# Optimization experiments

Hardware: AMD Instinct MI355X
Metric: run time of the kernel (lower is better)

The kernel has to match this reference:

```python
import jax, jax.numpy as jnp
import numpy as np

N_NODES = 50000
N_REL = 1000
N_EDGES = 1600000
F_OUT = 64
N_HEAD = 2
NEG_SLOPE = 0.2


def setup_inputs() -> dict:
    key = jax.random.key(0)
    k_h, k_r, k_a0, k_a1, k_a2, k_w, k_att = jax.random.split(key, 7)
    h = jax.random.normal(k_h, (N_NODES, F_OUT), dtype=jnp.float32)
    inputr = jax.random.normal(k_r, (N_REL, F_OUT), dtype=jnp.float32)
    # A[0]=dst node, A[1]=relation id, A[2]=src node
    a0 = jax.random.randint(k_a0, (N_EDGES,), 0, N_NODES, dtype=jnp.int32)
    a1 = jax.random.randint(k_a1, (N_EDGES,), 0, N_REL, dtype=jnp.int32)
    a2 = jax.random.randint(k_a2, (N_EDGES,), 0, N_NODES, dtype=jnp.int32)
    A = jnp.stack([a0, a1, a2], axis=0)
    # params: w ~ diag per-head scale, a_src_dst ~ N(0, 1/sqrt(2*f_out))
    w = jax.random.normal(k_w, (N_HEAD - 1, 1, F_OUT), dtype=jnp.float32)
    stdv = 1.0 / np.sqrt(2 * F_OUT)
    a_src_dst = (jax.random.normal(k_att, (N_HEAD, 2, F_OUT, 1), dtype=jnp.float32) * stdv)
    return {"h": h, "inputr": inputr, "A": A, "w": w, "a_src_dst": a_src_dst}


def reference(h, inputr, A, w, a_src_dst):
    N = h.shape[0]
    dst, rel_idx, src_idx = A[0], A[1], A[2]
    outs = []
    for i in range(N_HEAD):
        if i >= 1:
            h = h * w[i - 1]  # cumulative diag rescale across heads
        src = h[src_idx]          # [E, f] gather
        rel = inputr[rel_idx]     # [E, f] gather
        score = src @ a_src_dst[i, 0] + rel @ a_src_dst[i, 1]  # [E, 1]
        edge_e = jnp.exp(-jax.nn.leaky_relu(score[:, 0], NEG_SLOPE))  # [E]
        rowsum = jax.ops.segment_sum(edge_e, dst, num_segments=N)[:, None]  # [N,1]
        msg = (src - rel) * edge_e[:, None]  # [E, f]
        h_prime = jax.ops.segment_sum(msg, dst, num_segments=N) / rowsum
        outs.append(h_prime)
    return jnp.stack(outs, axis=0)  # [n_head, N, f]
```

## Files before the change

kernel.cpp:

```cpp
#include <hip/hip_runtime.h>
#include <hip/hip_fp16.h>

#define NNODES 50000
#define NREL   1000
#define NEDGES 1600000
#define FOUT   64
#define NEG_SLOPE 0.2f

#define SPAN   32
#define NBUCK  1563
#define CAP    1280
#define PTHR   1024
#define EPT    16
#define CHUNK  (PTHR * EPT)
#define DBLK   98
#define PREB   797


#define ALIGN1K(x) (((x) + 1023) & ~((size_t)1023))
static const size_t OFF_HS    = 0;
static const size_t OFF_RR    = ALIGN1K(OFF_HS    + sizeof(float2) * NNODES);
static const size_t OFF_CNT   = ALIGN1K(OFF_RR    + sizeof(float2) * NREL);
static const size_t OFF_H16   = ALIGN1K(OFF_CNT   + sizeof(int) * NBUCK);
static const size_t OFF_R16   = ALIGN1K(OFF_H16   + sizeof(unsigned short) * NNODES * FOUT);
static const size_t OFF_STAGE = ALIGN1K(OFF_R16   + sizeof(unsigned short) * NREL * FOUT);

__global__ __launch_bounds__(PTHR) void prep_kernel(
    const float* __restrict__ h, const float* __restrict__ inputr,
    const float* __restrict__ w, const float* __restrict__ a_att,
    const int* __restrict__ A, int* __restrict__ ccnt, int* __restrict__ stage,
    float2* __restrict__ hs2, float2* __restrict__ rr2,
    unsigned short* __restrict__ h16, unsigned short* __restrict__ r16)
{
    const int t = threadIdx.x;
    if (blockIdx.x < DBLK) {
        __shared__ int lcnt[NBUCK];
        __shared__ int gbase[NBUCK];
        for (int i = t; i < NBUCK; i += PTHR) lcnt[i] = 0;
        __syncthreads();

        const int base = blockIdx.x * CHUNK;
        int rec[EPT];
        short bkt[EPT];
        int off[EPT];

        #pragma unroll
        for (int k = 0; k < EPT; k++) {
            const int e = base + k * PTHR + t;
            if (e < NEDGES) {
                const int dn = __builtin_nontemporal_load(A + e);
                const int rn = __builtin_nontemporal_load(A + NEDGES + e);
                const int sn = __builtin_nontemporal_load(A + 2 * NEDGES + e);
                const int b  = dn >> 5;
                rec[k] = ((dn & 31) << 26) | (sn << 10) | rn;
                bkt[k] = (short)b;
                off[k] = atomicAdd(&lcnt[b], 1);
            } else {
                off[k] = -1;
            }
        }
        __syncthreads();

        for (int i = t; i < NBUCK; i += PTHR) {
            const int c = lcnt[i];
            if (c > 0) gbase[i] = i * CAP + atomicAdd(&ccnt[i], c);
        }
        __syncthreads();

        #pragma unroll
        for (int k = 0; k < EPT; k++) {
            if (off[k] >= 0) {
                const int b   = bkt[k];
                const int pos = gbase[b] + off[k];
                if (pos < (b + 1) * CAP)
                    stage[pos] = rec[k];
            }
        }
        return;
    }

    const int lane = t & 15;
    const int f0   = lane << 2;
    const int g    = (blockIdx.x - DBLK) * 64 + (t >> 4);
    if (g >= NNODES + NREL) return;

    const float4 a00 = *(const float4*)(a_att +   0 + f0);
    const float4 a01 = *(const float4*)(a_att +  64 + f0);
    const float4 a10 = *(const float4*)(a_att + 128 + f0);
    const float4 a11 = *(const float4*)(a_att + 192 + f0);
    const float4 wv  = *(const float4*)(w + f0);

    float p0, p1;
    float4 v;
    if (g < NNODES) {
        v = *(const float4*)(h + (size_t)g * FOUT + f0);
        p0 = v.x * a00.x + v.y * a00.y + v.z * a00.z + v.w * a00.w;
        p1 = v.x * wv.x * a10.x + v.y * wv.y * a10.y
           + v.z * wv.z * a10.z + v.w * wv.w * a10.w;
    } else {
        v = *(const float4*)(inputr + (size_t)(g - NNODES) * FOUT + f0);
        p0 = v.x * a01.x + v.y * a01.y + v.z * a01.z + v.w * a01.w;
        p1 = v.x * a11.x + v.y * a11.y + v.z * a11.z + v.w * a11.w;
    }

    {
        ushort4 pk;
        pk.x = __half_as_ushort(__float2half(v.x));
        pk.y = __half_as_ushort(__float2half(v.y));
        pk.z = __half_as_ushort(__float2half(v.z));
        pk.w = __half_as_ushort(__float2half(v.w));
        if (g < NNODES) *(ushort4*)(h16 + (size_t)g * FOUT + f0) = pk;
        else            *(ushort4*)(r16 + (size_t)(g - NNODES) * FOUT + f0) = pk;
    }

    #pragma unroll
    for (int off = 8; off >= 1; off >>= 1) {
        p0 += __shfl_xor(p0, off, 16);
        p1 += __shfl_xor(p1, off, 16);
    }
    if (lane == 0) {
        if (g < NNODES) hs2[g] = make_float2(p0, p1);
        else            rr2[g - NNODES] = make_float2(p0, p1);
    }
}

__global__ __launch_bounds__(256) void sortagg_kernel(
    const unsigned short* __restrict__ h16, const unsigned short* __restrict__ r16,
    const float* __restrict__ w,
    const int* __restrict__ stage, const int* __restrict__ ccnt,
    const float2* __restrict__ hs2, const float2* __restrict__ rr2,
    float* __restrict__ out)
{
    __shared__ int    lsort[CAP];
    __shared__ float2 ew[CAP];
    __shared__ int hist[SPAN];
    __shared__ int offs[SPAN];
    __shared__ int sstart[SPAN + 1];

    const int b = blockIdx.x;
    const int t = threadIdx.x;
    int cnt = ccnt[b];
    if (cnt > CAP) cnt = CAP;
    const int base = b * CAP;

    if (t < SPAN) hist[t] = 0;
    __syncthreads();

    for (int i = t; i < cnt; i += 256)
        atomicAdd(&hist[((unsigned)stage[base + i]) >> 26], 1);
    __syncthreads();

    if (t < SPAN) {
        const int c = hist[t];
        int v = c;
        #pragma unroll
        for (int d = 1; d < SPAN; d <<= 1) {
            const int u = __shfl_up(v, d);
            if (t >= d) v += u;
        }
        sstart[t] = v - c;
        offs[t]   = v - c;
        if (t == SPAN - 1) sstart[SPAN] = v;
    }
    __syncthreads();

    for (int i = t; i < cnt; i += 256) {
        const int r = stage[base + i];
        const int pos = atomicAdd(&offs[((unsigned)r) >> 26], 1);
        lsort[pos] = r;
        const int sn = (r >> 10) & 0xFFFF;
        const int rn = r & 1023;
        const float2 hv = hs2[sn];
        const float2 rv = rr2[rn];
        const float sc0 = hv.x + rv.x;
        const float sc1 = hv.y + rv.y;
        ew[pos] = make_float2(__expf(-fmaxf(sc0, NEG_SLOPE * sc0)),
                              __expf(-fmaxf(sc1, NEG_SLOPE * sc1)));
    }
    __syncthreads();

    const int wv = t >> 6;
    const int q  = (t & 63) >> 4;
    const int f4 = (t & 15) << 2;
    const float4 wl = *(const float4*)(w + f4);

    for (int nl = wv; nl < SPAN; nl += 4) {
        const int node = b * SPAN + nl;
        if (node >= NNODES) break;
        const int s0 = sstart[nl];
        const int s1 = sstart[nl + 1];

        float4 acc0 = make_float4(0.f, 0.f, 0.f, 0.f);
        float4 acc1 = make_float4(0.f, 0.f, 0.f, 0.f);
        float sum0 = 0.f, sum1 = 0.f;

        for (int i = s0 + q; i < s1; i += 4) {
            const int p     = lsort[i];
            const float2 ee = ew[i];
            const int sn = (p >> 10) & 0xFFFF;
            const int rn = p & 1023;

            const uint2 su = *(const uint2*)(h16 + ((size_t)sn << 6) + f4);
            const uint2 ru = *(const uint2*)(r16 + ((size_t)rn << 6) + f4);
            const float2 sxy = __half22float2(__builtin_bit_cast(__half2, su.x));
            const float2 szw = __half22float2(__builtin_bit_cast(__half2, su.y));
            const float2 rxy = __half22float2(__builtin_bit_cast(__half2, ru.x));
            const float2 rzw = __half22float2(__builtin_bit_cast(__half2, ru.y));

            acc0.x += (sxy.x - rxy.x) * ee.x;
            acc0.y += (sxy.y - rxy.y) * ee.x;
            acc0.z += (szw.x - rzw.x) * ee.x;
            acc0.w += (szw.y - rzw.y) * ee.x;
            acc1.x += fmaf(sxy.x, wl.x, -rxy.x) * ee.y;
            acc1.y += fmaf(sxy.y, wl.y, -rxy.y) * ee.y;
            acc1.z += fmaf(szw.x, wl.z, -rzw.x) * ee.y;
            acc1.w += fmaf(szw.y, wl.w, -rzw.y) * ee.y;
            sum0 += ee.x;
            sum1 += ee.y;
        }

        #pragma unroll
        for (int off = 16; off <= 32; off <<= 1) {
            acc0.x += __shfl_xor(acc0.x, off);
            acc0.y += __shfl_xor(acc0.y, off);
            acc0.z += __shfl_xor(acc0.z, off);
            acc0.w += __shfl_xor(acc0.w, off);
            acc1.x += __shfl_xor(acc1.x, off);
            acc1.y += __shfl_xor(acc1.y, off);
            acc1.z += __shfl_xor(acc1.z, off);
            acc1.w += __shfl_xor(acc1.w, off);
            sum0   += __shfl_xor(sum0, off);
            sum1   += __shfl_xor(sum1, off);
        }

        if (q == 0) {
            const float inv = 1.0f / sum0;
            float4 o = make_float4(acc0.x * inv, acc0.y * inv, acc0.z * inv, acc0.w * inv);
            *(float4*)(out + (size_t)node * FOUT + f4) = o;
        } else if (q == 1) {
            const float inv = 1.0f / sum1;
            float4 o = make_float4(acc1.x * inv, acc1.y * inv, acc1.z * inv, acc1.w * inv);
            *(float4*)(out + ((size_t)NNODES + node) * FOUT + f4) = o;
        }
    }
}

extern "C" void kernel_launch(void* const* d_in, const int* in_sizes, int n_in,
                              void* d_out, int out_size, void* d_ws, size_t ws_size,
                              hipStream_t stream) {
    const float* h      = (const float*)d_in[0];
    const float* inputr = (const float*)d_in[1];
    const int*   A      = (const int*)d_in[2];
    const float* w      = (const float*)d_in[3];
    const float* a_att  = (const float*)d_in[4];

    char* ws = (char*)d_ws;
    float2*         hs2   = (float2*)(ws + OFF_HS);
    float2*         rr2   = (float2*)(ws + OFF_RR);
    int*            ccnt  = (int*)(ws + OFF_CNT);
    unsigned short* h16   = (unsigned short*)(ws + OFF_H16);
    unsigned short* r16   = (unsigned short*)(ws + OFF_R16);
    int*            stage = (int*)(ws + OFF_STAGE);
    float*          out   = (float*)d_out;

    hipMemsetAsync(ccnt, 0, sizeof(int) * NBUCK, stream);

    prep_kernel<<<dim3(DBLK + PREB), dim3(PTHR), 0, stream>>>(
        h, inputr, w, a_att, A, ccnt, stage, hs2, rr2, h16, r16);
    sortagg_kernel<<<dim3(NBUCK), dim3(256), 0, stream>>>(
        h16, r16, w, stage, ccnt, hs2, rr2, out);
}
```

Measured before the change: 91.38 us.

## Halve destination bucket span and use 8-feature-per-lane gathers in aggregation

Destination buckets now cover 16 nodes instead of 32, which doubles the bucket count and lowers per-bucket capacity, so there are more and smaller aggregation blocks. In the aggregation loop each lane now loads 16-byte half-precision chunks covering 8 features. Eight edges are processed in parallel per wavefront instead of four, with an extra shuffle reduction step. The aim is more parallelism across the GPU and wider memory transactions, at the cost of more registers and more bucket-atomic contention in the prep stage. The node bounds check was dropped, which is safe only because 50000 divides evenly by 16.

New measurement: 88.45 us. 1.03x faster.

```diff
diff --git a/kernel.cpp b/kernel.cpp
--- a/kernel.cpp
+++ b/kernel.cpp
@@ -7,9 +7,9 @@
 #define FOUT   64
 #define NEG_SLOPE 0.2f
 
-#define SPAN   32
-#define NBUCK  1563
-#define CAP    1280
+#define SPAN   16
+#define NBUCK  3125
+#define CAP    704
 #define PTHR   1024
 #define EPT    16
 #define CHUNK  (PTHR * EPT)
@@ -51,8 +51,8 @@
                 const int dn = __builtin_nontemporal_load(A + e);
                 const int rn = __builtin_nontemporal_load(A + NEDGES + e);
                 const int sn = __builtin_nontemporal_load(A + 2 * NEDGES + e);
-                const int b  = dn >> 5;
-                rec[k] = ((dn & 31) << 26) | (sn << 10) | rn;
+                const int b  = dn >> 4;
+                rec[k] = ((dn & 15) << 26) | (sn << 10) | rn;
                 bkt[k] = (short)b;
                 off[k] = atomicAdd(&lcnt[b], 1);
             } else {
@@ -179,68 +179,92 @@
     }
     __syncthreads();
 
-    const int wv = t >> 6;
-    const int q  = (t & 63) >> 4;
-    const int f4 = (t & 15) << 2;
-    const float4 wl = *(const float4*)(w + f4);
+    const int wv  = t >> 6;
+    const int oct = (t & 63) >> 3;
+    const int f8  = (t & 7) << 3;
+    const float4 wl0 = *(const float4*)(w + f8);
+    const float4 wl1 = *(const float4*)(w + f8 + 4);
 
     for (int nl = wv; nl < SPAN; nl += 4) {
         const int node = b * SPAN + nl;
-        if (node >= NNODES) break;
         const int s0 = sstart[nl];
         const int s1 = sstart[nl + 1];
 
-        float4 acc0 = make_float4(0.f, 0.f, 0.f, 0.f);
-        float4 acc1 = make_float4(0.f, 0.f, 0.f, 0.f);
+        float4 a0l = make_float4(0.f, 0.f, 0.f, 0.f);
+        float4 a0h = make_float4(0.f, 0.f, 0.f, 0.f);
+        float4 a1l = make_float4(0.f, 0.f, 0.f, 0.f);
+        float4 a1h = make_float4(0.f, 0.f, 0.f, 0.f);
         float sum0 = 0.f, sum1 = 0.f;
 
-        for (int i = s0 + q; i < s1; i += 4) {
+        for (int i = s0 + oct; i < s1; i += 8) {
             const int p     = lsort[i];
             const float2 ee = ew[i];
             const int sn = (p >> 10) & 0xFFFF;
             const int rn = p & 1023;
 
-            const uint2 su = *(const uint2*)(h16 + ((size_t)sn << 6) + f4);
-            const uint2 ru = *(const uint2*)(r16 + ((size_t)rn << 6) + f4);
-            const float2 sxy = __half22float2(__builtin_bit_cast(__half2, su.x));
-            const float2 szw = __half22float2(__builtin_bit_cast(__half2, su.y));
-            const float2 rxy = __half22float2(__builtin_bit_cast(__half2, ru.x));
-            const float2 rzw = __half22float2(__builtin_bit_cast(__half2, ru.y));
-
-            acc0.x += (sxy.x - rxy.x) * ee.x;
-            acc0.y += (sxy.y - rxy.y) * ee.x;
-            acc0.z += (szw.x - rzw.x) * ee.x;
-            acc0.w += (szw.y - rzw.y) * ee.x;
-            acc1.x += fmaf(sxy.x, wl.x, -rxy.x) * ee.y;
-            acc1.y += fmaf(sxy.y, wl.y, -rxy.y) * ee.y;
-            acc1.z += fmaf(szw.x, wl.z, -rzw.x) * ee.y;
-            acc1.w += fmaf(szw.y, wl.w, -rzw.y) * ee.y;
+            const uint4 su = *(const uint4*)(h16 + ((size_t)sn << 6) + f8);
+            const uint4 ru = *(const uint4*)(r16 + ((size_t)rn << 6) + f8);
+            const float2 s01 = __half22float2(__builtin_bit_cast(__half2, su.x));
+            const float2 s23 = __half22float2(__builtin_bit_cast(__half2, su.y));
+            const float2 s45 = __half22float2(__builtin_bit_cast(__half2, su.z));
+            const float2 s67 = __half22float2(__builtin_bit_cast(__half2, su.w));
+            const float2 r01 = __half22float2(__builtin_bit_cast(__half2, ru.x));
+            const float2 r23 = __half22float2(__builtin_bit_cast(__half2, ru.y));
+            const float2 r45 = __half22float2(__builtin_bit_cast(__half2, ru.z));
+            const float2 r67 = __half22float2(__builtin_bit_cast(__half2, ru.w));
+
+            a0l.x += (s01.x - r01.x) * ee.x;
+            a0l.y += (s01.y - r01.y) * ee.x;
+            a0l.z += (s23.x - r23.x) * ee.x;
+            a0l.w += (s23.y - r23.y) * ee.x;
+            a0h.x += (s45.x - r45.x) * ee.x;
+            a0h.y += (s45.y - r45.y) * ee.x;
+            a0h.z += (s67.x - r67.x) * ee.x;
+            a0h.w += (s67.y - r67.y) * ee.x;
+            a1l.x += fmaf(s01.x, wl0.x, -r01.x) * ee.y;
+            a1l.y += fmaf(s01.y, wl0.y, -r01.y) * ee.y;
+            a1l.z += fmaf(s23.x, wl0.z, -r23.x) * ee.y;
+            a1l.w += fmaf(s23.y, wl0.w, -r23.y) * ee.y;
+            a1h.x += fmaf(s45.x, wl1.x, -r45.x) * ee.y;
+            a1h.y += fmaf(s45.y, wl1.y, -r45.y) * ee.y;
+            a1h.z += fmaf(s67.x, wl1.z, -r67.x) * ee.y;
+            a1h.w += fmaf(s67.y, wl1.w, -r67.y) * ee.y;
             sum0 += ee.x;
             sum1 += ee.y;
         }
 
         #pragma unroll
-        for (int off = 16; off <= 32; off <<= 1) {
-            acc0.x += __shfl_xor(acc0.x, off);
-            acc0.y += __shfl_xor(acc0.y, off);
-            acc0.z += __shfl_xor(acc0.z, off);
-            acc0.w += __shfl_xor(acc0.w, off);
-            acc1.x += __shfl_xor(acc1.x, off);
-            acc1.y += __shfl_xor(acc1.y, off);
-            acc1.z += __shfl_xor(acc1.z, off);
-            acc1.w += __shfl_xor(acc1.w, off);
+        for (int off = 8; off <= 32; off <<= 1) {
+            a0l.x += __shfl_xor(a0l.x, off);
+            a0l.y += __shfl_xor(a0l.y, off);
+            a0l.z += __shfl_xor(a0l.z, off);
+            a0l.w += __shfl_xor(a0l.w, off);
+            a0h.x += __shfl_xor(a0h.x, off);
+            a0h.y += __shfl_xor(a0h.y, off);
+            a0h.z += __shfl_xor(a0h.z, off);
+            a0h.w += __shfl_xor(a0h.w, off);
+            a1l.x += __shfl_xor(a1l.x, off);
+            a1l.y += __shfl_xor(a1l.y, off);
+            a1l.z += __shfl_xor(a1l.z, off);
+            a1l.w += __shfl_xor(a1l.w, off);
+            a1h.x += __shfl_xor(a1h.x, off);
+            a1h.y += __shfl_xor(a1h.y, off);
+            a1h.z += __shfl_xor(a1h.z, off);
+            a1h.w += __shfl_xor(a1h.w, off);
             sum0   += __shfl_xor(sum0, off);
             sum1   += __shfl_xor(sum1, off);
         }
 
-        if (q == 0) {
+        if (oct == 0) {
             const float inv = 1.0f / sum0;
-            float4 o = make_float4(acc0.x * inv, acc0.y * inv, acc0.z * inv, acc0.w * inv);
-            *(float4*)(out + (size_t)node * FOUT + f4) = o;
-        } else if (q == 1) {
+            float* o = out + (size_t)node * FOUT + f8;
+            *(float4*)(o)     = make_float4(a0l.x * inv, a0l.y * inv, a0l.z * inv, a0l.w * inv);
+            *(float4*)(o + 4) = make_float4(a0h.x * inv, a0h.y * inv, a0h.z * inv, a0h.w * inv);
+        } else if (oct == 1) {
             const float inv = 1.0f / sum1;
-            float4 o = make_float4(acc1.x * inv, acc1.y * inv, acc1.z * inv, acc1.w * inv);
-            *(float4*)(out + ((size_t)NNODES + node) * FOUT + f4) = o;
+            float* o = out + ((size_t)NNODES + node) * FOUT + f8;
+            *(float4*)(o)     = make_float4(a1l.x * inv, a1l.y * inv, a1l.z * inv, a1l.w * inv);
+            *(float4*)(o + 4) = make_float4(a1h.x * inv, a1h.y * inv, a1h.z * inv, a1h.w * inv);
         }
     }
 }
```
